# Kernel tuning notes

Measured on AMD Instinct MI355X. Metric: run time of the kernel, lower is better.

The kernel has to match this reference:

```python
import jax, jax.numpy as jnp
import numpy as np

D_EMBED = 1024
D_HIDDEN = 1024
BATCH = 8192


def setup_inputs() -> dict:
    key = jax.random.key(0)
    ks = jax.random.split(key, 11)
    din = D_EMBED + D_HIDDEN
    s = 1.0 / np.sqrt(din)  # torch Linear default init scale
    def lin(kw, kb):
        W = jax.random.uniform(kw, (din, D_HIDDEN), minval=-s, maxval=s, dtype=jnp.float32)
        b = jax.random.uniform(kb, (D_HIDDEN,), minval=-s, maxval=s, dtype=jnp.float32)
        return W, b
    Wf, bf = lin(ks[0], ks[1])
    Wi, bi = lin(ks[2], ks[3])
    Wo, bo = lin(ks[4], ks[5])
    Wu, bu = lin(ks[6], ks[7])
    x = jax.random.normal(ks[8], (BATCH, D_EMBED), dtype=jnp.float32)
    h = jax.random.normal(ks[9], (BATCH, D_HIDDEN), dtype=jnp.float32)
    c = jax.random.normal(ks[10], (BATCH, D_HIDDEN), dtype=jnp.float32)
    return {"x": x, "h": h, "c": c,
            "Wf": Wf, "bf": bf, "Wi": Wi, "bi": bi,
            "Wo": Wo, "bo": bo, "Wu": Wu, "bu": bu}


def reference(x, h, c, Wf, bf, Wi, bi, Wo, bo, Wu, bu):
    xh = jnp.concatenate([x, h], axis=-1)              # [B, d_embed+d_hidden]
    # Fused gate GEMM: concat weights along output dim -> one [B, 4H] matmul.
    W = jnp.concatenate([Wf, Wi, Wo, Wu], axis=1)      # [din, 4H]
    b = jnp.concatenate([bf, bi, bo, bu], axis=0)      # [4H]
    gates = xh @ W + b                                 # [B, 4H]
    f, i, o, u = jnp.split(gates, 4, axis=-1)
    f = jax.nn.sigmoid(f)
    i = jax.nn.sigmoid(i)
    o = jax.nn.sigmoid(o)
    c_hat = jnp.tanh(u)
    new_c = f * c + i * c_hat
    new_h = o * jnp.tanh(new_c)
    return (new_h, new_c)
```

## Files before the change

### kernel.cpp

```cpp
#include <hip/hip_runtime.h>
#include <hip/hip_bf16.h>

#define BATCH 8192
#define DK    2048
#define DH    1024
#define DN    4096
#define NT    64

typedef __attribute__((ext_vector_type(8))) short bf16x8;
typedef __attribute__((ext_vector_type(4))) short short4v;
typedef __attribute__((ext_vector_type(4))) float f32x4;

__device__ __forceinline__ unsigned short f2bf(float f) {
    union { float f; unsigned u; } v; v.f = f;
    unsigned r = v.u + 0x7FFFu + ((v.u >> 16) & 1u);
    return (unsigned short)(r >> 16);
}
__device__ __forceinline__ float sigm(float x)  { return 1.0f / (1.0f + __expf(-x)); }
__device__ __forceinline__ float tanh_(float x) { return 1.0f - 2.0f / (1.0f + __expf(2.0f * x)); }

__device__ __forceinline__ void glds16(const void* g, void* l) {
    __builtin_amdgcn_global_load_lds(
        (const __attribute__((address_space(1))) unsigned*)g,
        (__attribute__((address_space(3))) unsigned*)l, 16, 0, 0);
}

__global__ void cvtA_k(const float* __restrict__ x, const float* __restrict__ h,
                       short* __restrict__ A) {
    long t = (long)blockIdx.x * 256 + threadIdx.x;
    long idx = t << 3;
    long b   = idx >> 10;
    int  col = (int)(idx & 1023);
    {
        float4 v0 = *(const float4*)(x + idx);
        float4 v1 = *(const float4*)(x + idx + 4);
        bf16x8 s;
        s[0]=(short)f2bf(v0.x); s[1]=(short)f2bf(v0.y); s[2]=(short)f2bf(v0.z); s[3]=(short)f2bf(v0.w);
        s[4]=(short)f2bf(v1.x); s[5]=(short)f2bf(v1.y); s[6]=(short)f2bf(v1.z); s[7]=(short)f2bf(v1.w);
        *(bf16x8*)(A + b * DK + col) = s;
    }
    {
        float4 v0 = *(const float4*)(h + idx);
        float4 v1 = *(const float4*)(h + idx + 4);
        bf16x8 s;
        s[0]=(short)f2bf(v0.x); s[1]=(short)f2bf(v0.y); s[2]=(short)f2bf(v0.z); s[3]=(short)f2bf(v0.w);
        s[4]=(short)f2bf(v1.x); s[5]=(short)f2bf(v1.y); s[6]=(short)f2bf(v1.z); s[7]=(short)f2bf(v1.w);
        *(bf16x8*)(A + b * DK + 1024 + col) = s;
    }
}

__global__ void cvtW_k(const float* __restrict__ W0, const float* __restrict__ W1,
                       const float* __restrict__ W2, const float* __restrict__ W3,
                       short* __restrict__ Wt) {
    __shared__ float tile[64][65];
    const int g = blockIdx.z;
    const float* Wg = (g == 0) ? W0 : (g == 1) ? W1 : (g == 2) ? W2 : W3;
    int k0 = blockIdx.x << 6;
    int j0 = blockIdx.y << 6;
    int tid = threadIdx.x;
    int rr = tid >> 4, c4 = (tid & 15) << 2;
#pragma unroll
    for (int i = 0; i < 4; i++) {
        int r = rr + (i << 4);
        float4 v = *(const float4*)(Wg + (long)(k0 + r) * DH + j0 + c4);
        tile[r][c4] = v.x; tile[r][c4+1] = v.y; tile[r][c4+2] = v.z; tile[r][c4+3] = v.w;
    }
    __syncthreads();
#pragma unroll
    for (int i = 0; i < 4; i++) {
        int jr = rr + (i << 4);
        int j  = j0 + jr;
        int n  = ((j >> 4) << 6) + (g << 4) + (j & 15);
        short4v s;
        s[0]=(short)f2bf(tile[c4+0][jr]); s[1]=(short)f2bf(tile[c4+1][jr]);
        s[2]=(short)f2bf(tile[c4+2][jr]); s[3]=(short)f2bf(tile[c4+3][jr]);
        *(short4v*)(Wt + (long)n * DK + k0 + c4) = s;
    }
}

__launch_bounds__(512, 1)
__global__ void gemm_k(const short* __restrict__ A, const short* __restrict__ W,
                       const float* __restrict__ cin,
                       const float* __restrict__ bfv, const float* __restrict__ biv,
                       const float* __restrict__ bov, const float* __restrict__ buv,
                       float* __restrict__ out) {
    __shared__ char sA[65536];
    __shared__ char sB[65536];

    const int bid = blockIdx.x;
    const int wg  = ((bid & 7) << 6) + (bid >> 3);
    const int nt  = wg >> 5;
    const int mt  = wg & 31;
    const int tid = threadIdx.x;
    const int lane = tid & 63;
    const int wv = tid >> 6;
    const int wr = wv >> 2;
    const int wc = wv & 3;

    const int srow  = tid >> 2;
    const int sslot = (tid & 3) ^ ((tid >> 3) & 3);
    const long a0 = (long)(mt * 256 + srow)       * DK + sslot * 8;
    const long a1 = (long)(mt * 256 + 128 + srow) * DK + sslot * 8;
    const long b0 = (long)(nt * 256 + srow)       * DK + sslot * 8;
    const long b1 = (long)(nt * 256 + 128 + srow) * DK + sslot * 8;

    int offA[8], offB[4];
#pragma unroll
    for (int i = 0; i < 8; i++) {
        int rA = (wr << 7) + (i << 4) + (lane & 15);
        offA[i] = (rA << 6) + (((lane >> 4) ^ ((rA >> 1) & 3)) << 4);
    }
#pragma unroll
    for (int g = 0; g < 4; g++) {
        int rB = (wc << 6) + (g << 4) + (lane & 15);
        offB[g] = (rB << 6) + (((lane >> 4) ^ ((rB >> 1) & 3)) << 4);
    }

    f32x4 acc[8][4];
    const f32x4 fz = {0.f, 0.f, 0.f, 0.f};
#pragma unroll
    for (int i = 0; i < 8; i++)
#pragma unroll
        for (int g = 0; g < 4; g++) acc[i][g] = fz;

    auto STAGE = [&](int t) {
        const int buf = t & 3;
        char* la = sA + (buf << 14) + (tid << 4);
        char* lb = sB + (buf << 14) + (tid << 4);
        const long ko = (long)t << 5;
        glds16(A + a0 + ko, la);
        glds16(A + a1 + ko, la + 8192);
        glds16(W + b0 + ko, lb);
        glds16(W + b1 + ko, lb + 8192);
    };

    auto BODY = [&](int t, bool doStage, int vml) {
        const int bo2 = (t & 3) << 14;
        if (doStage) STAGE(t + 3);
        bf16x8 bv[4], av[4];
#pragma unroll
        for (int g = 0; g < 4; g++) bv[g] = *(const bf16x8*)(sB + bo2 + offB[g]);
#pragma unroll
        for (int i = 0; i < 4; i++) av[i] = *(const bf16x8*)(sA + bo2 + offA[i]);
        __builtin_amdgcn_s_setprio(1);
#pragma unroll
        for (int i = 0; i < 4; i++)
#pragma unroll
            for (int g = 0; g < 4; g++)
                acc[i][g] = __builtin_amdgcn_mfma_f32_16x16x32_bf16(av[i], bv[g], acc[i][g], 0, 0, 0);
        __builtin_amdgcn_s_setprio(0);
#pragma unroll
        for (int i = 0; i < 4; i++) av[i] = *(const bf16x8*)(sA + bo2 + offA[i + 4]);
        __builtin_amdgcn_s_setprio(1);
#pragma unroll
        for (int i = 0; i < 4; i++)
#pragma unroll
            for (int g = 0; g < 4; g++)
                acc[i + 4][g] = __builtin_amdgcn_mfma_f32_16x16x32_bf16(av[i], bv[g], acc[i + 4][g], 0, 0, 0);
        __builtin_amdgcn_s_setprio(0);
        if (vml == 8)      asm volatile("s_waitcnt vmcnt(8)" ::: "memory");
        else if (vml == 4) asm volatile("s_waitcnt vmcnt(4)" ::: "memory");
        else if (vml == 0) asm volatile("s_waitcnt vmcnt(0)" ::: "memory");
        if (vml >= 0) __builtin_amdgcn_s_barrier();
    };

    STAGE(0); STAGE(1); STAGE(2);
    asm volatile("s_waitcnt vmcnt(8)" ::: "memory");
    __builtin_amdgcn_s_barrier();

#pragma unroll 1
    for (int t = 0; t <= NT - 4; ++t) BODY(t, true, 8);
    BODY(NT - 3, false, 4);
    BODY(NT - 2, false, 0);
    BODY(NT - 1, false, -1);

    const int hid = nt * 64 + wc * 16 + (lane & 15);
    const long rowb = (long)mt * 256 + (wr << 7) + ((lane >> 4) << 2);
    const float b_f = bfv[hid], b_i = biv[hid], b_o = bov[hid], b_u = buv[hid];
#pragma unroll
    for (int i = 0; i < 8; i++) {
#pragma unroll
        for (int q = 0; q < 4; q++) {
            const long r = rowb + (i << 4) + q;
            float f  = sigm(acc[i][0][q] + b_f);
            float i_ = sigm(acc[i][1][q] + b_i);
            float o_ = sigm(acc[i][2][q] + b_o);
            float u_ = tanh_(acc[i][3][q] + b_u);
            float nc = f * cin[r * DH + hid] + i_ * u_;
            out[r * DH + hid] = o_ * tanh_(nc);
            out[(long)BATCH * DH + r * DH + hid] = nc;
        }
    }
}

__global__ void naive_k(const float* __restrict__ x, const float* __restrict__ h,
                        const float* __restrict__ cin,
                        const float* __restrict__ Wf, const float* __restrict__ bfv,
                        const float* __restrict__ Wi, const float* __restrict__ biv,
                        const float* __restrict__ Wo, const float* __restrict__ bov,
                        const float* __restrict__ Wu, const float* __restrict__ buv,
                        float* __restrict__ out) {
    long t = (long)blockIdx.x * 256 + threadIdx.x;
    long b = t >> 10; int j = (int)(t & 1023);
    float sf = bfv[j], si = biv[j], so = bov[j], su = buv[j];
    for (int k = 0; k < 1024; k++) {
        float xv = x[b * 1024 + k];
        long w = (long)k * 1024 + j;
        sf += xv * Wf[w]; si += xv * Wi[w]; so += xv * Wo[w]; su += xv * Wu[w];
    }
    for (int k = 0; k < 1024; k++) {
        float hv = h[b * 1024 + k];
        long w = (long)(k + 1024) * 1024 + j;
        sf += hv * Wf[w]; si += hv * Wi[w]; so += hv * Wo[w]; su += hv * Wu[w];
    }
    float f = sigm(sf), i_ = sigm(si), o_ = sigm(so), u_ = tanh_(su);
    float nc = f * cin[t] + i_ * u_;
    out[t] = o_ * tanh_(nc);
    out[(long)BATCH * DH + t] = nc;
}

extern "C" void kernel_launch(void* const* d_in, const int* in_sizes, int n_in,
                              void* d_out, int out_size, void* d_ws, size_t ws_size,
                              hipStream_t stream) {
    const float* x   = (const float*)d_in[0];
    const float* h   = (const float*)d_in[1];
    const float* c   = (const float*)d_in[2];
    const float* Wf  = (const float*)d_in[3];
    const float* bf_ = (const float*)d_in[4];
    const float* Wi  = (const float*)d_in[5];
    const float* bi_ = (const float*)d_in[6];
    const float* Wo  = (const float*)d_in[7];
    const float* bo_ = (const float*)d_in[8];
    const float* Wu  = (const float*)d_in[9];
    const float* bu_ = (const float*)d_in[10];
    float* out = (float*)d_out;

    const size_t needA = (size_t)BATCH * DK * 2;
    const size_t needW = (size_t)DN * DK * 2;

    if (ws_size < needA + needW) {
        naive_k<<<(BATCH * DH) / 256, 256, 0, stream>>>(x, h, c, Wf, bf_, Wi, bi_, Wo, bo_, Wu, bu_, out);
        return;
    }

    short* Abf = (short*)d_ws;
    short* Wt  = (short*)((char*)d_ws + needA);

    cvtA_k<<<(BATCH * DH) / (256 * 8), 256, 0, stream>>>(x, h, Abf);
    cvtW_k<<<dim3(DK / 64, DH / 64, 4), 256, 0, stream>>>(Wf, Wi, Wo, Wu, Wt);
    gemm_k<<<512, 512, 0, stream>>>(Abf, Wt, c, bf_, bi_, bo_, bu_, out);
}
```

Measured before the change: 354.2 us.

## Split global-to-LDS staging across MFMA phases with ping-pong barriers

Splits the per-iteration global-to-LDS prefetch into separate A and B halves. The A half is issued before the first MFMA block and the B half before the second, and each phase is fenced with sched_barrier, s_barrier and lgkmcnt waits. The intent is to interleave memory issue with matrix math in a ping-pong schedule, so waves stay synchronised and loads spread out instead of bursting. In exchange it adds two extra workgroup barriers per K step, which could stall waves and reduce latency hiding.

```diff
diff --git a/kernel.cpp b/kernel.cpp
--- a/kernel.cpp
+++ b/kernel.cpp
@@ -123,25 +123,31 @@
 #pragma unroll
         for (int g = 0; g < 4; g++) acc[i][g] = fz;
 
-    auto STAGE = [&](int t) {
-        const int buf = t & 3;
-        char* la = sA + (buf << 14) + (tid << 4);
-        char* lb = sB + (buf << 14) + (tid << 4);
+    auto STAGEA = [&](int t) {
+        char* la = sA + ((t & 3) << 14) + (tid << 4);
         const long ko = (long)t << 5;
         glds16(A + a0 + ko, la);
         glds16(A + a1 + ko, la + 8192);
+    };
+    auto STAGEB = [&](int t) {
+        char* lb = sB + ((t & 3) << 14) + (tid << 4);
+        const long ko = (long)t << 5;
         glds16(W + b0 + ko, lb);
         glds16(W + b1 + ko, lb + 8192);
     };
 
     auto BODY = [&](int t, bool doStage, int vml) {
         const int bo2 = (t & 3) << 14;
-        if (doStage) STAGE(t + 3);
         bf16x8 bv[4], av[4];
+        if (doStage) STAGEA(t + 3);
 #pragma unroll
         for (int g = 0; g < 4; g++) bv[g] = *(const bf16x8*)(sB + bo2 + offB[g]);
 #pragma unroll
         for (int i = 0; i < 4; i++) av[i] = *(const bf16x8*)(sA + bo2 + offA[i]);
+        __builtin_amdgcn_sched_barrier(0);
+        __builtin_amdgcn_s_barrier();
+        asm volatile("s_waitcnt lgkmcnt(0)" ::: "memory");
+        __builtin_amdgcn_sched_barrier(0);
         __builtin_amdgcn_s_setprio(1);
 #pragma unroll
         for (int i = 0; i < 4; i++)
@@ -149,8 +155,16 @@
             for (int g = 0; g < 4; g++)
                 acc[i][g] = __builtin_amdgcn_mfma_f32_16x16x32_bf16(av[i], bv[g], acc[i][g], 0, 0, 0);
         __builtin_amdgcn_s_setprio(0);
+        __builtin_amdgcn_sched_barrier(0);
+        __builtin_amdgcn_s_barrier();
+        __builtin_amdgcn_sched_barrier(0);
+        if (doStage) STAGEB(t + 3);
 #pragma unroll
         for (int i = 0; i < 4; i++) av[i] = *(const bf16x8*)(sA + bo2 + offA[i + 4]);
+        __builtin_amdgcn_sched_barrier(0);
+        __builtin_amdgcn_s_barrier();
+        asm volatile("s_waitcnt lgkmcnt(0)" ::: "memory");
+        __builtin_amdgcn_sched_barrier(0);
         __builtin_amdgcn_s_setprio(1);
 #pragma unroll
         for (int i = 0; i < 4; i++)
@@ -158,15 +172,20 @@
             for (int g = 0; g < 4; g++)
                 acc[i + 4][g] = __builtin_amdgcn_mfma_f32_16x16x32_bf16(av[i], bv[g], acc[i + 4][g], 0, 0, 0);
         __builtin_amdgcn_s_setprio(0);
+        __builtin_amdgcn_sched_barrier(0);
         if (vml == 8)      asm volatile("s_waitcnt vmcnt(8)" ::: "memory");
         else if (vml == 4) asm volatile("s_waitcnt vmcnt(4)" ::: "memory");
         else if (vml == 0) asm volatile("s_waitcnt vmcnt(0)" ::: "memory");
-        if (vml >= 0) __builtin_amdgcn_s_barrier();
+        if (vml >= 0) {
+            __builtin_amdgcn_s_barrier();
+            __builtin_amdgcn_sched_barrier(0);
+        }
     };
 
-    STAGE(0); STAGE(1); STAGE(2);
+    STAGEA(0); STAGEB(0); STAGEA(1); STAGEB(1); STAGEA(2); STAGEB(2);
     asm volatile("s_waitcnt vmcnt(8)" ::: "memory");
     __builtin_amdgcn_s_barrier();
+    __builtin_amdgcn_sched_barrier(0);
 
 #pragma unroll 1
     for (int t = 0; t <= NT - 4; ++t) BODY(t, true, 8);
```

New measurement: 348.6 us. Within noise of the previous version (-1.6%).
